# Kernel optimization log

Measured on AMD Instinct MI355X. Metric: run time of the kernel, lower is better.

## Reference

```python
import jax, jax.numpy as jnp
import numpy as np

B, FIELD, H_PREV, H_NEXT = 4096, 128, 128, 256


def setup_inputs() -> dict:
    key = jax.random.key(0)
    k0, k1, k2, k3 = jax.random.split(key, 4)
    x0 = jax.random.normal(k0, (B, FIELD), dtype=jnp.float32)
    x = jax.random.normal(k1, (B, H_PREV), dtype=jnp.float32)
    # Conv1d(1, H_NEXT, kernel=stride=H_PREV*FIELD) weight, reshaped so that
    # flat index k = f*H_PREV + p  ->  W[o, f, p]
    fan_in = H_PREV * FIELD
    bound = 1.0 / np.sqrt(fan_in)
    W = jax.random.uniform(k2, (H_NEXT, FIELD, H_PREV), dtype=jnp.float32, minval=-bound, maxval=bound)
    b = jax.random.uniform(k3, (H_NEXT,), dtype=jnp.float32, minval=-bound, maxval=bound)
    return {"x0": x0, "x": x, "W": W, "b": b}


def reference(x0, x, W, b):
    # outer product x0[b,f]*x[b,p] flattened then full-window conv == bilinear form
    outer = x0[:, :, None] * x[:, None, :]            # [B, FIELD, H_PREV]
    out = jnp.einsum('bfp,ofp->bo', outer, W) + b      # [B, H_NEXT]
    return out[:, :, None]                             # [B, H_NEXT, 1] like Conv1d output
```

## Files before the change

kernel.cpp:

```cpp
#include <hip/hip_runtime.h>


typedef _Float16 f16x8 __attribute__((ext_vector_type(8)));
typedef float    f32x4 __attribute__((ext_vector_type(4)));

#define WS_WT_OFF  0
#define WS_XF_OFF  8388608
#define WS_X0_OFF  9437184
#define WS_NEEDED  10485760

__device__ __forceinline__ void gl_lds16(const void* g, void* l) {
  __builtin_amdgcn_global_load_lds(
      (const __attribute__((address_space(1))) void*)g,
      (__attribute__((address_space(3))) void*)l, 16, 0, 0);
}

__global__ __launch_bounds__(256) void prep_kernel(
    const float* __restrict__ x0, const float* __restrict__ x,
    const float* __restrict__ W, _Float16* __restrict__ WT2,
    _Float16* __restrict__ Xf, _Float16* __restrict__ X0T2)
{
  int i = blockIdx.x * 256 + threadIdx.x;
  if (i < 524288) {
    int o = i >> 11, k8 = i & 2047;
    const float* s = W + ((size_t)o << 14) + ((size_t)k8 << 3);
    f16x8 h;
#pragma unroll
    for (int e = 0; e < 8; ++e) h[e] = (_Float16)s[e];
    int ks = k8 >> 2, g = k8 & 3, ob = o >> 6, o6 = o & 63;
    int wv = ks >> 6, r = ks & 63, f = r >> 2, q = r & 3;
    int widx = q * 16 + f;
    *(f16x8*)(WT2 + ((size_t)((ob * 512 + wv * 64 + widx) * 4 + g)) * 512 +
              o6 * 8) = h;
  } else if (i < 589824) {
    int j = i - 524288;
    int r = j >> 4, seg = j & 15;
    const float* s = x + r * 128 + seg * 8;
    f16x8 h;
#pragma unroll
    for (int e = 0; e < 8; ++e) h[e] = (_Float16)s[e];
    int segp = seg ^ (r & 7);
    *(f16x8*)(Xf + r * 128 + segp * 8) = h;
  } else {
    int j = i - 589824;
    int mb = j >> 10, rem = j & 1023;
    int row = rem >> 4, jb = rem & 15;
    f16x8 h;
#pragma unroll
    for (int e = 0; e < 8; ++e)
      h[e] = (_Float16)x0[(size_t)(mb * 64 + row) * 128 + jb * 8 + e];
    *(f16x8*)(X0T2 + (size_t)mb * 8192 + row * 128 + (jb ^ (row & 7)) * 8) = h;
  }
}

__global__ __launch_bounds__(512, 2) void gemm_kernel(
    const _Float16* __restrict__ WT2, const _Float16* __restrict__ Xf,
    const _Float16* __restrict__ X0T2, const float* __restrict__ bias,
    float* __restrict__ out)
{
  __shared__ __align__(16) char smem[139264];

  const int bid = blockIdx.x;
  const int mb  = bid >> 2;
  const int ob  = bid & 3;

  const int t  = threadIdx.x;
  const int l  = t & 63;
  const int wv = t >> 6;
  const int lr = l & 15;
  const int lg = l >> 4;
  const int swz = lr & 7;

  const char* wsrc = (const char*)WT2 + ((size_t)(ob * 512 + wv * 64)) * 4096;
  const int wofs = lg * 1024 + lr * 16;

  const char* xsb = (const char*)Xf + (size_t)mb * 16384;
  gl_lds16(xsb + 0 * 8192 + t * 16, smem + 0 * 8192 + t * 16);
  gl_lds16(xsb + 1 * 8192 + t * 16, smem + 1 * 8192 + t * 16);
  const char* x0b = (const char*)X0T2 + (size_t)mb * 16384;
  gl_lds16(x0b + 0 * 8192 + t * 16, smem + 16384 + 0 * 8192 + t * 16);
  gl_lds16(x0b + 1 * 8192 + t * 16, smem + 16384 + 1 * 8192 + t * 16);
  __syncthreads();

  f32x4 acc[4][4] = {};
  f16x8 xa[4], x0v[4], bw0[4], bw1[4], bw2[4];

#pragma unroll
  for (int m = 0; m < 4; ++m)
    xa[m] = *(const f16x8*)(smem + (m * 16 + lr) * 256 + ((lg ^ swz) << 4));
#pragma unroll
  for (int m = 0; m < 4; ++m)
    x0v[m] = *(const f16x8*)(smem + 16384 + (m * 16 + lr) * 256 +
                             (((wv * 2) ^ swz) << 4));
#pragma unroll
  for (int i = 0; i < 4; ++i)
    bw0[i] = *(const f16x8*)(wsrc + 0 * 4096 + i * 256 + wofs);
#pragma unroll
  for (int i = 0; i < 4; ++i)
    bw1[i] = *(const f16x8*)(wsrc + 1 * 4096 + i * 256 + wofs);

#define STEP(WI, BR, BW_, STG) { \
    if (STG) { \
      _Pragma("unroll") \
      for (int i = 0; i < 4; ++i) \
        BW_[i] = *(const f16x8*)(wsrc + ((WI) + 2) * 4096 + i * 256 + wofs); \
    } \
    f16x8 av[4]; \
    _Pragma("unroll") \
    for (int m = 0; m < 4; ++m) \
      av[m] = xa[m] * x0v[m][(WI) & 7]; \
    if ((((WI) + 1) & 15) == 0 && (WI) < 63) { \
      _Pragma("unroll") \
      for (int m = 0; m < 4; ++m) \
        xa[m] = *(const f16x8*)(smem + (m * 16 + lr) * 256 + \
                 ((((((WI) + 1) >> 4) * 4 + lg) ^ swz) << 4)); \
    } \
    if ((((WI) + 1) & 7) == 0 && (WI) < 63) { \
      _Pragma("unroll") \
      for (int m = 0; m < 4; ++m) \
        x0v[m] = *(const f16x8*)(smem + 16384 + (m * 16 + lr) * 256 + \
                  (((wv * 2 + ((((WI) + 1) >> 3) & 1)) ^ swz) << 4)); \
    } \
    _Pragma("unroll") \
    for (int m = 0; m < 4; ++m) { \
      _Pragma("unroll") \
      for (int n = 0; n < 4; ++n) \
        acc[m][n] = __builtin_amdgcn_mfma_f32_16x16x32_f16( \
            av[m], BR[n], acc[m][n], 0, 0, 0); \
    } \
  }

#define S0(WI, STG) STEP(WI, bw0, bw2, STG)
#define S1(WI, STG) STEP(WI, bw1, bw0, STG)
#define S2(WI, STG) STEP(WI, bw2, bw1, STG)

  S0(0,1)  S1(1,1)  S2(2,1)  S0(3,1)  S1(4,1)  S2(5,1)
  S0(6,1)  S1(7,1)  S2(8,1)  S0(9,1)  S1(10,1) S2(11,1)
  S0(12,1) S1(13,1) S2(14,1) S0(15,1) S1(16,1) S2(17,1)
  S0(18,1) S1(19,1) S2(20,1) S0(21,1) S1(22,1) S2(23,1)
  S0(24,1) S1(25,1) S2(26,1) S0(27,1) S1(28,1) S2(29,1)
  S0(30,1) S1(31,1) S2(32,1) S0(33,1) S1(34,1) S2(35,1)
  S0(36,1) S1(37,1) S2(38,1) S0(39,1) S1(40,1) S2(41,1)
  S0(42,1) S1(43,1) S2(44,1) S0(45,1) S1(46,1) S2(47,1)
  S0(48,1) S1(49,1) S2(50,1) S0(51,1) S1(52,1) S2(53,1)
  S0(54,1) S1(55,1) S2(56,1) S0(57,1) S1(58,1) S2(59,1)
  S0(60,1) S1(61,1) S2(62,0) S0(63,0)

#undef S0
#undef S1
#undef S2
#undef STEP

  __syncthreads();

#pragma unroll
  for (int m = 0; m < 4; ++m)
#pragma unroll
    for (int n = 0; n < 4; ++n)
      *(f32x4*)(smem + wv * 17408 + (n * 16 + lr) * 272 +
                (m * 16 + lg * 4) * 4) = acc[m][n];

  __syncthreads();

  {
    const int row = t >> 3, c8 = (t & 7) * 8;
    float v[8];
#pragma unroll
    for (int c = 0; c < 8; ++c) {
      float s = 0.f;
#pragma unroll
      for (int w = 0; w < 8; ++w)
        s += *(const float*)(smem + w * 17408 + (c8 + c) * 272 + row * 4);
      v[c] = s;
    }
    const float4 b0 = *(const float4*)(bias + ob * 64 + c8);
    const float4 b1 = *(const float4*)(bias + ob * 64 + c8 + 4);
    float* op = out + (size_t)(mb * 64 + row) * 256 + ob * 64 + c8;
    float4 o0 = {v[0] + b0.x, v[1] + b0.y, v[2] + b0.z, v[3] + b0.w};
    float4 o1 = {v[4] + b1.x, v[5] + b1.y, v[6] + b1.z, v[7] + b1.w};
    *(float4*)(op)     = o0;
    *(float4*)(op + 4) = o1;
  }
}

__global__ __launch_bounds__(256) void naive_kernel(
    const float* __restrict__ x0, const float* __restrict__ x,
    const float* __restrict__ W, const float* __restrict__ bias,
    float* __restrict__ out)
{
  __shared__ float x0_s[16][128];
  __shared__ float x_s[16][128];
  const int tid = threadIdx.x;
  const int b0  = blockIdx.x * 16;
  for (int i = tid; i < 16 * 128; i += 256) {
    int bb = i >> 7, c = i & 127;
    x0_s[bb][c] = x0[(size_t)(b0 + bb) * 128 + c];
    x_s[bb][c]  = x[(size_t)(b0 + bb) * 128 + c];
  }
  __syncthreads();
  const int lane = tid & 63, wv = tid >> 6;
  for (int o = wv; o < 256; o += 4) {
    float acc[16];
#pragma unroll
    for (int bb = 0; bb < 16; ++bb) acc[bb] = 0.f;
    for (int it = 0; it < 256; ++it) {
      int k = it * 64 + lane;
      float wval = W[(size_t)o * 16384 + k];
      int f = k >> 7, p = k & 127;
#pragma unroll
      for (int bb = 0; bb < 16; ++bb)
        acc[bb] += wval * (x0_s[bb][f] * x_s[bb][p]);
    }
#pragma unroll
    for (int bb = 0; bb < 16; ++bb) {
      float v = acc[bb];
      for (int off = 32; off; off >>= 1) v += __shfl_down(v, off);
      if (lane == 0) out[(size_t)(b0 + bb) * 256 + o] = v + bias[o];
    }
  }
}

extern "C" void kernel_launch(void* const* d_in, const int* in_sizes, int n_in,
                              void* d_out, int out_size, void* d_ws,
                              size_t ws_size, hipStream_t stream)
{
  const float* x0   = (const float*)d_in[0];
  const float* x    = (const float*)d_in[1];
  const float* W    = (const float*)d_in[2];
  const float* bias = (const float*)d_in[3];
  float* out = (float*)d_out;

  if (ws_size >= (size_t)WS_NEEDED) {
    _Float16* WT2  = (_Float16*)((char*)d_ws + WS_WT_OFF);
    _Float16* Xf   = (_Float16*)((char*)d_ws + WS_XF_OFF);
    _Float16* X0T2 = (_Float16*)((char*)d_ws + WS_X0_OFF);
    prep_kernel<<<2560, 256, 0, stream>>>(x0, x, W, WT2, Xf, X0T2);
    gemm_kernel<<<256, 512, 0, stream>>>(WT2, Xf, X0T2, bias, out);
  } else {
    naive_kernel<<<256, 256, 0, stream>>>(x0, x, W, bias, out);
  }
}
```

Before: 49.16 us.

## Split-K gemm across four blocks with atomic output accumulation and bias pre-init

The gemm grid grows from 256 to 1024 blocks by splitting the K dimension into four slices per (mb, ob) tile, with smaller 256-thread blocks, half the output columns per wave and much less LDS so more blocks fit per CU. The cross-wave LDS reduction and its two barriers are dropped. Each wave now atomically adds its partial sums straight into the output, which the prep kernel pre-fills with the bias. Weights are repacked into a new layout that matches the split. This trades a larger number of float atomics to global memory, and an extra output-init pass in prep, for more parallelism and occupancy.

```diff
diff --git a/kernel.cpp b/kernel.cpp
--- a/kernel.cpp
+++ b/kernel.cpp
@@ -17,8 +17,9 @@
 
 __global__ __launch_bounds__(256) void prep_kernel(
     const float* __restrict__ x0, const float* __restrict__ x,
-    const float* __restrict__ W, _Float16* __restrict__ WT2,
-    _Float16* __restrict__ Xf, _Float16* __restrict__ X0T2)
+    const float* __restrict__ W, const float* __restrict__ bias,
+    char* __restrict__ WT3, _Float16* __restrict__ Xf,
+    _Float16* __restrict__ X0T2, float* __restrict__ out)
 {
   int i = blockIdx.x * 256 + threadIdx.x;
   if (i < 524288) {
@@ -27,11 +28,11 @@
     f16x8 h;
 #pragma unroll
     for (int e = 0; e < 8; ++e) h[e] = (_Float16)s[e];
-    int ks = k8 >> 2, g = k8 & 3, ob = o >> 6, o6 = o & 63;
-    int wv = ks >> 6, r = ks & 63, f = r >> 2, q = r & 3;
-    int widx = q * 16 + f;
-    *(f16x8*)(WT2 + ((size_t)((ob * 512 + wv * 64 + widx) * 4 + g)) * 512 +
-              o6 * 8) = h;
+    int ob = o >> 6, oh = (o >> 5) & 1, n = (o >> 4) & 1;
+    int l  = (o & 15) | ((k8 & 3) << 4);
+    int sk = k8 >> 9, kh = (k8 >> 8) & 1, fi = (k8 >> 4) & 15, q = (k8 >> 2) & 3;
+    size_t widx = (size_t)((((ob * 2 + oh) * 4 + sk) * 2 + kh) * 64 + q * 16 + fi);
+    *(f16x8*)(WT3 + widx * 2048 + n * 1024 + l * 16) = h;
   } else if (i < 589824) {
     int j = i - 524288;
     int r = j >> 4, seg = j & 15;
@@ -41,7 +42,7 @@
     for (int e = 0; e < 8; ++e) h[e] = (_Float16)s[e];
     int segp = seg ^ (r & 7);
     *(f16x8*)(Xf + r * 128 + segp * 8) = h;
-  } else {
+  } else if (i < 655360) {
     int j = i - 589824;
     int mb = j >> 10, rem = j & 1023;
     int row = rem >> 4, jb = rem & 15;
@@ -50,40 +51,49 @@
     for (int e = 0; e < 8; ++e)
       h[e] = (_Float16)x0[(size_t)(mb * 64 + row) * 128 + jb * 8 + e];
     *(f16x8*)(X0T2 + (size_t)mb * 8192 + row * 128 + (jb ^ (row & 7)) * 8) = h;
-  }
-}
-
-__global__ __launch_bounds__(512, 2) void gemm_kernel(
-    const _Float16* __restrict__ WT2, const _Float16* __restrict__ Xf,
-    const _Float16* __restrict__ X0T2, const float* __restrict__ bias,
-    float* __restrict__ out)
-{
-  __shared__ __align__(16) char smem[139264];
+  } else {
+    int j = i - 655360;
+    int c = (j * 4) & 255;
+    ((float4*)out)[j] = *(const float4*)(bias + c);
+  }
+}
+
+__global__ __launch_bounds__(256, 4) void gemm_kernel(
+    const char* __restrict__ WT3, const _Float16* __restrict__ Xf,
+    const _Float16* __restrict__ X0T2, float* __restrict__ out)
+{
+  __shared__ __align__(16) char smem[32768];
 
   const int bid = blockIdx.x;
-  const int mb  = bid >> 2;
+  const int mb  = bid >> 4;
+  const int sk  = (bid >> 2) & 3;
   const int ob  = bid & 3;
 
-  const int t  = threadIdx.x;
-  const int l  = t & 63;
-  const int wv = t >> 6;
-  const int lr = l & 15;
-  const int lg = l >> 4;
+  const int t   = threadIdx.x;
+  const int l   = t & 63;
+  const int wv  = t >> 6;
+  const int oh  = wv & 1;
+  const int kh  = wv >> 1;
+  const int lr  = l & 15;
+  const int lg  = l >> 4;
   const int swz = lr & 7;
-
-  const char* wsrc = (const char*)WT2 + ((size_t)(ob * 512 + wv * 64)) * 4096;
-  const int wofs = lg * 1024 + lr * 16;
+  const int l16 = l * 16;
+
+  const char* wbase = WT3 +
+      (size_t)((((ob * 2 + oh) * 4 + sk) * 2 + kh) * 64) * 2048;
 
   const char* xsb = (const char*)Xf + (size_t)mb * 16384;
-  gl_lds16(xsb + 0 * 8192 + t * 16, smem + 0 * 8192 + t * 16);
-  gl_lds16(xsb + 1 * 8192 + t * 16, smem + 1 * 8192 + t * 16);
+#pragma unroll
+  for (int i = 0; i < 4; ++i)
+    gl_lds16(xsb + i * 4096 + t * 16, smem + i * 4096 + t * 16);
   const char* x0b = (const char*)X0T2 + (size_t)mb * 16384;
-  gl_lds16(x0b + 0 * 8192 + t * 16, smem + 16384 + 0 * 8192 + t * 16);
-  gl_lds16(x0b + 1 * 8192 + t * 16, smem + 16384 + 1 * 8192 + t * 16);
+#pragma unroll
+  for (int i = 0; i < 4; ++i)
+    gl_lds16(x0b + i * 4096 + t * 16, smem + 16384 + i * 4096 + t * 16);
   __syncthreads();
 
-  f32x4 acc[4][4] = {};
-  f16x8 xa[4], x0v[4], bw0[4], bw1[4], bw2[4];
+  f32x4 acc[4][2] = {};
+  f16x8 xa[4], x0v[4], bw0[2], bw1[2], bw2[2];
 
 #pragma unroll
   for (int m = 0; m < 4; ++m)
@@ -91,19 +101,19 @@
 #pragma unroll
   for (int m = 0; m < 4; ++m)
     x0v[m] = *(const f16x8*)(smem + 16384 + (m * 16 + lr) * 256 +
-                             (((wv * 2) ^ swz) << 4));
-#pragma unroll
-  for (int i = 0; i < 4; ++i)
-    bw0[i] = *(const f16x8*)(wsrc + 0 * 4096 + i * 256 + wofs);
-#pragma unroll
-  for (int i = 0; i < 4; ++i)
-    bw1[i] = *(const f16x8*)(wsrc + 1 * 4096 + i * 256 + wofs);
+                             (((sk * 4 + kh * 2) ^ swz) << 4));
+#pragma unroll
+  for (int i = 0; i < 2; ++i)
+    bw0[i] = *(const f16x8*)(wbase + 0 * 2048 + i * 1024 + l16);
+#pragma unroll
+  for (int i = 0; i < 2; ++i)
+    bw1[i] = *(const f16x8*)(wbase + 1 * 2048 + i * 1024 + l16);
 
 #define STEP(WI, BR, BW_, STG) { \
     if (STG) { \
       _Pragma("unroll") \
-      for (int i = 0; i < 4; ++i) \
-        BW_[i] = *(const f16x8*)(wsrc + ((WI) + 2) * 4096 + i * 256 + wofs); \
+      for (int i = 0; i < 2; ++i) \
+        BW_[i] = *(const f16x8*)(wbase + ((WI) + 2) * 2048 + i * 1024 + l16); \
     } \
     f16x8 av[4]; \
     _Pragma("unroll") \
@@ -119,12 +129,12 @@
       _Pragma("unroll") \
       for (int m = 0; m < 4; ++m) \
         x0v[m] = *(const f16x8*)(smem + 16384 + (m * 16 + lr) * 256 + \
-                  (((wv * 2 + ((((WI) + 1) >> 3) & 1)) ^ swz) << 4)); \
+                  (((sk * 4 + kh * 2 + ((((WI) + 1) >> 3) & 1)) ^ swz) << 4)); \
     } \
     _Pragma("unroll") \
     for (int m = 0; m < 4; ++m) { \
       _Pragma("unroll") \
-      for (int n = 0; n < 4; ++n) \
+      for (int n = 0; n < 2; ++n) \
         acc[m][n] = __builtin_amdgcn_mfma_f32_16x16x32_f16( \
             av[m], BR[n], acc[m][n], 0, 0, 0); \
     } \
@@ -151,36 +161,15 @@
 #undef S2
 #undef STEP
 
-  __syncthreads();
-
+  float* op = out + (size_t)(mb * 64 + lg * 4) * 256 + ob * 64 + oh * 32 + lr;
 #pragma unroll
   for (int m = 0; m < 4; ++m)
 #pragma unroll
-    for (int n = 0; n < 4; ++n)
-      *(f32x4*)(smem + wv * 17408 + (n * 16 + lr) * 272 +
-                (m * 16 + lg * 4) * 4) = acc[m][n];
-
-  __syncthreads();
-
-  {
-    const int row = t >> 3, c8 = (t & 7) * 8;
-    float v[8];
-#pragma unroll
-    for (int c = 0; c < 8; ++c) {
-      float s = 0.f;
-#pragma unroll
-      for (int w = 0; w < 8; ++w)
-        s += *(const float*)(smem + w * 17408 + (c8 + c) * 272 + row * 4);
-      v[c] = s;
-    }
-    const float4 b0 = *(const float4*)(bias + ob * 64 + c8);
-    const float4 b1 = *(const float4*)(bias + ob * 64 + c8 + 4);
-    float* op = out + (size_t)(mb * 64 + row) * 256 + ob * 64 + c8;
-    float4 o0 = {v[0] + b0.x, v[1] + b0.y, v[2] + b0.z, v[3] + b0.w};
-    float4 o1 = {v[4] + b1.x, v[5] + b1.y, v[6] + b1.z, v[7] + b1.w};
-    *(float4*)(op)     = o0;
-    *(float4*)(op + 4) = o1;
-  }
+    for (int n = 0; n < 2; ++n)
+#pragma unroll
+      for (int rr = 0; rr < 4; ++rr)
+        unsafeAtomicAdd(op + (size_t)(m * 16 + rr) * 256 + n * 16,
+                        acc[m][n][rr]);
 }
 
 __global__ __launch_bounds__(256) void naive_kernel(
@@ -231,11 +220,11 @@
   float* out = (float*)d_out;
 
   if (ws_size >= (size_t)WS_NEEDED) {
-    _Float16* WT2  = (_Float16*)((char*)d_ws + WS_WT_OFF);
+    char*     WT3  = (char*)d_ws + WS_WT_OFF;
     _Float16* Xf   = (_Float16*)((char*)d_ws + WS_XF_OFF);
     _Float16* X0T2 = (_Float16*)((char*)d_ws + WS_X0_OFF);
-    prep_kernel<<<2560, 256, 0, stream>>>(x0, x, W, WT2, Xf, X0T2);
-    gemm_kernel<<<256, 512, 0, stream>>>(WT2, Xf, X0T2, bias, out);
+    prep_kernel<<<3584, 256, 0, stream>>>(x0, x, W, bias, WT3, Xf, X0T2, out);
+    gemm_kernel<<<1024, 256, 0, stream>>>(WT3, Xf, X0T2, out);
   } else {
     naive_kernel<<<256, 256, 0, stream>>>(x0, x, W, bias, out);
   }
```

Measured after the change: 66.36 us. 1.35x slower.
